# Performance work log

Hardware: AMD Instinct MI355X
Metric: run time of the kernel (lower is better)

Reference implementation:

```python
import jax, jax.numpy as jnp
from jax import lax
import numpy as np

T = 8
TAU = 2.0       # LIFNode tau
VTH = 1.0       # v_threshold for IF and LIF
ALPHA = 2.0     # surrogate.ATan default alpha
BN_EPS = 1e-5

# --- ATan surrogate-gradient heaviside (spikingjelly semantics) ---
@jax.custom_vjp
def heaviside_atan(x):
    return (x >= 0.0).astype(x.dtype)

def _h_fwd(x):
    return heaviside_atan(x), x

def _h_bwd(x, g):
    sg = (ALPHA / 2.0) / (1.0 + (jnp.pi / 2.0 * ALPHA * x) ** 2)
    return (g * sg,)

heaviside_atan.defvjp(_h_fwd, _h_bwd)

# --- multi-step IF node: v += x; spike; hard reset to 0 ---
def if_node(x_seq):
    def step(v, x):
        v = v + x
        s = heaviside_atan(v - VTH)
        return (1.0 - s) * v, s
    return lax.scan(step, jnp.zeros_like(x_seq[0]), x_seq)[1]

# --- multi-step LIF node (decay_input=True, v_reset=0, hard reset) ---
def lif_node(x_seq):
    def step(v, x):
        v = v + (x - v) / TAU
        s = heaviside_atan(v - VTH)
        return (1.0 - s) * v, s
    return lax.scan(step, jnp.zeros_like(x_seq[0]), x_seq)[1]

def conv2d(x, w, b):
    y = lax.conv_general_dilated(x, w, (1, 1), 'SAME', dimension_numbers=('NCHW', 'OIHW', 'NCHW'))
    return y + b[None, :, None, None]

def bn(x, g, b, m, v):
    scale = g * lax.rsqrt(v + BN_EPS)
    return (x - m[None, :, None, None]) * scale[None, :, None, None] + b[None, :, None, None]

def maxpool2(x):
    return lax.reduce_window(x, -jnp.inf, lax.max, (1, 1, 2, 2), (1, 1, 2, 2), 'VALID')


def setup_inputs():
    key = jax.random.key(0)
    ks = jax.random.split(key, 8)
    B = 32
    f32 = jnp.float32
    d = {}
    d['x'] = jax.random.normal(ks[0], (B, 1, 48, 48), f32)
    d['conv1_w'] = jax.random.normal(ks[1], (128, 1, 3, 3), f32) * 0.2
    d['conv1_b'] = jnp.zeros((128,), f32)
    d['bn1_g'] = jnp.ones((128,), f32)
    d['bn1_b'] = jnp.zeros((128,), f32)
    d['bn1_m'] = jnp.zeros((128,), f32)
    d['bn1_v'] = jnp.ones((128,), f32)
    d['conv2_w'] = jax.random.normal(ks[2], (128, 128, 3, 3), f32) * 0.03
    d['conv2_b'] = jnp.zeros((128,), f32)
    d['bn2_g'] = jnp.ones((128,), f32)
    d['bn2_b'] = jnp.zeros((128,), f32)
    d['bn2_m'] = jnp.zeros((128,), f32)
    d['bn2_v'] = jnp.ones((128,), f32)
    d['fc1_w'] = jax.random.normal(ks[3], (1152, 128 * 12 * 12), f32) * 0.007
    d['fc1_b'] = jnp.zeros((1152,), f32)
    d['fc2_w'] = jax.random.normal(ks[4], (128, 1152), f32) * 0.03
    d['fc2_b'] = jnp.zeros((128,), f32)
    d['fc3_w'] = jax.random.normal(ks[5], (7, 128), f32) * 0.09
    d['fc3_b'] = jnp.zeros((7,), f32)
    return d


def reference(x, conv1_w, conv1_b, bn1_g, bn1_b, bn1_m, bn1_v,
              conv2_w, conv2_b, bn2_g, bn2_b, bn2_m, bn2_v,
              fc1_w, fc1_b, fc2_w, fc2_b, fc3_w, fc3_b):
    B = x.shape[0]
    # layer1 (single-step): conv + BN (eval-mode), dropout is identity at eval
    h = bn(conv2d(x, conv1_w, conv1_b), bn1_g, bn1_b, bn1_m, bn1_v)  # [B,128,48,48]
    # repeat over T timesteps
    x_step = jnp.broadcast_to(h, (T,) + h.shape)                      # [T,B,128,48,48]
    # layer2: IF -> maxpool -> conv -> BN -> IF -> maxpool
    s1 = if_node(x_step)                                              # [T,B,128,48,48]
    p1 = maxpool2(s1.reshape((T * B,) + s1.shape[2:]))                # [T*B,128,24,24]
    c2 = bn(conv2d(p1, conv2_w, conv2_b), bn2_g, bn2_b, bn2_m, bn2_v)
    s2 = if_node(c2.reshape((T, B) + c2.shape[1:]))                   # [T,B,128,24,24]
    p2 = maxpool2(s2.reshape((T * B,) + s2.shape[2:]))                # [T*B,128,12,12]
    # layer3: flatten -> fc -> LIF -> fc -> LIF -> fc -> LIF
    f = p2.reshape(T, B, -1)                                          # [T,B,18432]
    l1 = lif_node(jnp.einsum('tbi,oi->tbo', f, fc1_w) + fc1_b)        # [T,B,1152]
    l2 = lif_node(jnp.einsum('tbi,oi->tbo', l1, fc2_w) + fc2_b)       # [T,B,128]
    l3 = lif_node(jnp.einsum('tbi,oi->tbo', l2, fc3_w) + fc3_b)       # [T,B,7]
    return l3.mean(axis=0)                                            # [B,7]
```

## Files before the change

### kernel.cpp

```cpp
#include <hip/hip_runtime.h>
#include <hip/hip_bf16.h>


typedef float  f32x4  __attribute__((ext_vector_type(4)));
typedef __bf16 bf16x8 __attribute__((ext_vector_type(8)));

#define T_STEPS 8

static const size_t OFF_P1    = 0;
static const size_t OFF_PART  = 0;
static const size_t OFF_WT    = 44302336;
static const size_t OFF_P2    = 45481984;
static const size_t OFF_W2T   = 54919168;
static const size_t OFF_L1S   = 55508992;

__device__ __forceinline__ unsigned short bf16_rne(float f) {
  unsigned u = __builtin_bit_cast(unsigned, f);
  u += 0x7FFFu + ((u >> 16) & 1u);
  return (unsigned short)(u >> 16);
}
__device__ __forceinline__ float bf16_to_f(unsigned short h) {
  unsigned u = ((unsigned)h) << 16;
  return __builtin_bit_cast(float, u);
}

__device__ __forceinline__ void split_pair(float f0, float f1, unsigned& hi, unsigned& lo) {
  __hip_bfloat162 h2 = __float22bfloat162_rn(make_float2(f0, f1));
  unsigned uh; __builtin_memcpy(&uh, &h2, 4);
  float g0 = __builtin_bit_cast(float, uh << 16);
  float g1 = __builtin_bit_cast(float, uh & 0xFFFF0000u);
  __hip_bfloat162 l2 = __float22bfloat162_rn(make_float2(f0 - g0, f1 - g1));
  unsigned ul; __builtin_memcpy(&ul, &l2, 4);
  hi = uh;
  lo = ul;
}

__device__ __forceinline__ void lds_load16(const void* g, void* l) {
  auto* gp = reinterpret_cast<const __attribute__((address_space(1))) unsigned int*>(
      reinterpret_cast<uintptr_t>(g));
  auto* lp = reinterpret_cast<__attribute__((address_space(3))) unsigned int*>(
      reinterpret_cast<uintptr_t>(l));
  __builtin_amdgcn_global_load_lds(gp, lp, 16, 0, 0);
}

__global__ __launch_bounds__(256) void prep(const float* __restrict__ conv2_w,
                                            const float* __restrict__ fc2_w,
                                            short* __restrict__ wt_hi,
                                            short* __restrict__ wt_lo,
                                            float* __restrict__ w2t,
                                            uint4* __restrict__ p1pad4) {
  int i = blockIdx.x * 256 + threadIdx.x;
  if (i < 147456) {
    int tap = i >> 14;
    int oc  = (i >> 7) & 127;
    int ic  = i & 127;
    float wv = conv2_w[oc * 1152 + ic * 9 + tap];
    unsigned short h = bf16_rne(wv);
    wt_hi[i] = (short)h;
    wt_lo[i] = (short)bf16_rne(wv - bf16_to_f(h));
  } else if (i < 294912) {
    int j = i - 147456;
    int o = j & 127, k = j >> 7;
    w2t[j] = fc2_w[o * 1152 + k];
  } else if (i < 704512) {
    int k = i - 294912;
    int tb = k / 1600;
    int rem = k - tb * 1600;
    int pos = rem >> 4, c8 = rem & 15;
    int y, x;
    if (pos < 26)      { y = 0;  x = pos; }
    else if (pos < 52) { y = 25; x = pos - 26; }
    else { int jj = pos - 52; y = 1 + (jj >> 1); x = (jj & 1) * 25; }
    p1pad4[(tb * 676 + y * 26 + x) * 16 + c8] = make_uint4(0u, 0u, 0u, 0u);
  }
}

__global__ __launch_bounds__(128) void conv1_if_pool(
    const float* __restrict__ x, const float* __restrict__ w1, const float* __restrict__ b1,
    const float* __restrict__ g1, const float* __restrict__ be1, const float* __restrict__ m1,
    const float* __restrict__ vv1, short* __restrict__ p1) {
  __shared__ float patch[16];
  const int c  = threadIdx.x;
  const int sp = blockIdx.x;
  const int b  = blockIdx.y;
  const int oy = sp / 24, ox = sp % 24;
  if (c < 16) {
    int py = c >> 2, px = c & 3;
    int iy = 2 * oy - 1 + py, ix = 2 * ox - 1 + px;
    float v = 0.f;
    if (iy >= 0 && iy < 48 && ix >= 0 && ix < 48) v = x[b * 2304 + iy * 48 + ix];
    patch[c] = v;
  }
  __syncthreads();
  float w[9];
#pragma unroll
  for (int i = 0; i < 9; ++i) w[i] = w1[c * 9 + i];
  float scale = g1[c] * rsqrtf(vv1[c] + 1e-5f);
  float shift = (b1[c] - m1[c]) * scale + be1[c];
  float h[4];
#pragma unroll
  for (int p = 0; p < 4; ++p) {
    int py = p >> 1, px = p & 1;
    float s = 0.f;
#pragma unroll
    for (int dy = 0; dy < 3; ++dy)
#pragma unroll
      for (int dx = 0; dx < 3; ++dx) s += patch[(py + dy) * 4 + (px + dx)] * w[dy * 3 + dx];
    h[p] = s * scale + shift;
  }
  float va = 0.f, vb = 0.f, vc = 0.f, vd = 0.f;
  size_t base = ((size_t)b * 676 + (size_t)(1 + oy) * 26 + (1 + ox)) * 128 + c;
#pragma unroll
  for (int t = 0; t < T_STEPS; ++t) {
    va += h[0]; vb += h[1]; vc += h[2]; vd += h[3];
    bool s0 = va >= 1.f, s1 = vb >= 1.f, s2 = vc >= 1.f, s3 = vd >= 1.f;
    p1[base + (size_t)t * (32 * 676 * 128)] = (s0 | s1 | s2 | s3) ? (short)0x3F80 : (short)0;
    if (s0) va = 0.f; if (s1) vb = 0.f; if (s2) vc = 0.f; if (s3) vd = 0.f;
  }
}

__global__ __launch_bounds__(256, 2) void conv2_gemm(
    const short* __restrict__ p1pad, const short* __restrict__ wt_hi, const short* __restrict__ wt_lo,
    const float* __restrict__ conv2_b, const float* __restrict__ bn2_g, const float* __restrict__ bn2_b,
    const float* __restrict__ bn2_m, const float* __restrict__ bn2_v, short* __restrict__ p2) {
  __shared__ __align__(16) short lds[32768];
  short* ldsA  = lds;
  short* ldsBh = lds + 16384;
  short* ldsBl = lds + 24576;

  const int tid = threadIdx.x;
  const int lane = tid & 63;
  const int w = tid >> 6;
  const int wm = w & 1, wn = w >> 1;
  const int b = blockIdx.y;
  const int gy = blockIdx.x / 3;
  const int gx = blockIdx.x - gy * 3;

  const int g = (lane & 7) ^ (lane >> 3);
  int rowofsA[8], bofs[4];
#pragma unroll
  for (int j = 0; j < 8; ++j) {
    int r = w * 64 + j * 8 + (lane >> 3);
    int t = r >> 5, iy = (r >> 3) & 3, ix = r & 7;
    rowofsA[j] = (((t * 32 + b) * 676) + (4 * gy + iy) * 26 + (8 * gx + ix)) * 128 + g * 8;
  }
#pragma unroll
  for (int j = 0; j < 4; ++j) {
    int n = w * 32 + j * 8 + (lane >> 3);
    bofs[j] = n * 128 + g * 8;
  }

  f32x4 acc[8][4];
#pragma unroll
  for (int mi = 0; mi < 8; ++mi)
#pragma unroll
    for (int ni = 0; ni < 4; ++ni) acc[mi][ni] = (f32x4){0.f, 0.f, 0.f, 0.f};

#pragma unroll 1
  for (int s = 0; s < 18; ++s) {
    const int tap = s >> 1;
    const int kk = (s & 1) << 6;
    const int tapoff = ((tap / 3) * 26 + (tap % 3)) * 128;
    __syncthreads();
#pragma unroll
    for (int j = 0; j < 8; ++j) {
      lds_load16(p1pad + rowofsA[j] + tapoff + kk, ldsA + (w * 64 + j * 8) * 64 + lane * 8);
    }
    const int wtoff = tap * 16384 + kk;
#pragma unroll
    for (int j = 0; j < 4; ++j) {
      lds_load16(wt_hi + wtoff + bofs[j], ldsBh + (w * 32 + j * 8) * 64 + lane * 8);
      lds_load16(wt_lo + wtoff + bofs[j], ldsBl + (w * 32 + j * 8) * 64 + lane * 8);
    }
    __syncthreads();
#pragma unroll
    for (int ks = 0; ks < 2; ++ks) {
      const int cch = ks * 4 + (lane >> 4);
      bf16x8 a[8], bh[4], bl[4];
#pragma unroll
      for (int i = 0; i < 8; ++i) {
        int r = wm * 128 + i * 16 + (lane & 15);
        a[i] = *(const bf16x8*)(ldsA + r * 64 + ((cch ^ (r & 7)) * 8));
      }
#pragma unroll
      for (int i = 0; i < 4; ++i) {
        int n = wn * 64 + i * 16 + (lane & 15);
        bh[i] = *(const bf16x8*)(ldsBh + n * 64 + ((cch ^ (n & 7)) * 8));
        bl[i] = *(const bf16x8*)(ldsBl + n * 64 + ((cch ^ (n & 7)) * 8));
      }
#pragma unroll
      for (int mi = 0; mi < 8; ++mi)
#pragma unroll
        for (int ni = 0; ni < 4; ++ni) {
          acc[mi][ni] = __builtin_amdgcn_mfma_f32_16x16x32_bf16(a[mi], bh[ni], acc[mi][ni], 0, 0, 0);
          acc[mi][ni] = __builtin_amdgcn_mfma_f32_16x16x32_bf16(a[mi], bl[ni], acc[mi][ni], 0, 0, 0);
        }
    }
  }

  float sc[4], sh[4];
#pragma unroll
  for (int ni = 0; ni < 4; ++ni) {
    int oc = wn * 64 + ni * 16 + (lane & 15);
    sc[ni] = bn2_g[oc] * rsqrtf(bn2_v[oc] + 1e-5f);
    sh[ni] = (conv2_b[oc] - bn2_m[oc]) * sc[ni] + bn2_b[oc];
  }
  float* ybuf = (float*)lds;
  const int S = 132;
  float v[32];
#pragma unroll
  for (int q = 0; q < 32; ++q) v[q] = 0.f;
  unsigned short* p2u = (unsigned short*)p2;
  __syncthreads();
#pragma unroll
  for (int q = 0; q < 4; ++q) {
    if (wm == (q >> 1)) {
      const int mib = (q & 1) * 4;
#pragma unroll
      for (int ml = 0; ml < 4; ++ml)
#pragma unroll
        for (int ni = 0; ni < 4; ++ni)
#pragma unroll
          for (int r = 0; r < 4; ++r) {
            int lam = ml * 16 + ((lane >> 4) << 2) + r;
            int col = wn * 64 + ni * 16 + (lane & 15);
            ybuf[lam * S + col] = acc[mib + ml][ni][r] * sc[ni] + sh[ni];
          }
    }
    __syncthreads();
    if (tid < 128) {
      const int oc = tid;
#pragma unroll
      for (int tt = 0; tt < 2; ++tt) {
        int t = 2 * q + tt;
#pragma unroll
        for (int pooly = 0; pooly < 2; ++pooly) {
          unsigned short ov[4];
#pragma unroll
          for (int poolx = 0; poolx < 4; ++poolx) {
            bool any = false;
#pragma unroll
            for (int ry = 0; ry < 2; ++ry)
#pragma unroll
              for (int rx = 0; rx < 2; ++rx) {
                int iy = 2 * pooly + ry, ix = 2 * poolx + rx;
                float xx = ybuf[(tt * 32 + iy * 8 + ix) * S + oc];
                int qi = iy * 8 + ix;
                v[qi] += xx;
                bool ss = v[qi] >= 1.f;
                any |= ss;
                if (ss) v[qi] = 0.f;
              }
            ov[poolx] = any ? (unsigned short)0x3F80 : (unsigned short)0;
          }
          ushort4 o4; o4.x = ov[0]; o4.y = ov[1]; o4.z = ov[2]; o4.w = ov[3];
          *(ushort4*)(p2u + ((size_t)(t * 32 + b) * 128 + oc) * 144 + (2 * gy + pooly) * 12 + 4 * gx) = o4;
        }
      }
    }
    __syncthreads();
  }
}

__global__ __launch_bounds__(512) void fc1_gemm(const short* __restrict__ p2,
                                                const float* __restrict__ fc1_w,
                                                float* __restrict__ part) {
  __shared__ __align__(16) short lds[32768];
  short* ldsA = lds;
  short* ldsBh = lds + 16384;
  short* ldsBl = lds + 24576;

  const int tid = threadIdx.x;
  const int lane = tid & 63;
  const int w = tid >> 6;
  const int wm = w & 3, wn = w >> 2;
  const int n0 = blockIdx.x * 128;
  const int kb = blockIdx.y * 576;

  const int g = (lane & 7) ^ (lane >> 3);
  int aofs[4];
#pragma unroll
  for (int j = 0; j < 4; ++j) {
    int r = w * 32 + j * 8 + (lane >> 3);
    aofs[j] = r * 18432 + g * 8;
  }
  const int bn = tid >> 2;
  const int c0 = (tid & 3) * 2;
  const float* wrow = fc1_w + (size_t)(n0 + bn) * 18432 + c0 * 8;
  const int bpos0 = (c0 ^ (bn & 7)) * 8;
  const int bpos1 = ((c0 + 1) ^ (bn & 7)) * 8;

  f32x4 acc[4][4];
#pragma unroll
  for (int mi = 0; mi < 4; ++mi)
#pragma unroll
    for (int ni = 0; ni < 4; ++ni) acc[mi][ni] = (f32x4){0.f, 0.f, 0.f, 0.f};

#pragma unroll 1
  for (int s = 0; s < 9; ++s) {
    const int koff = kb + s * 64;
    __syncthreads();
#pragma unroll
    for (int j = 0; j < 4; ++j) {
      lds_load16(p2 + aofs[j] + koff, ldsA + (w * 32 + j * 8) * 64 + lane * 8);
    }
    {
      const float4* wp = (const float4*)(wrow + koff);
      float4 q0 = wp[0], q1 = wp[1], q2 = wp[2], q3 = wp[3];
      unsigned h0, h1, h2, h3, h4, h5, h6, h7;
      unsigned l0, l1, l2, l3, l4, l5, l6, l7;
      split_pair(q0.x, q0.y, h0, l0);
      split_pair(q0.z, q0.w, h1, l1);
      split_pair(q1.x, q1.y, h2, l2);
      split_pair(q1.z, q1.w, h3, l3);
      split_pair(q2.x, q2.y, h4, l4);
      split_pair(q2.z, q2.w, h5, l5);
      split_pair(q3.x, q3.y, h6, l6);
      split_pair(q3.z, q3.w, h7, l7);
      uint4 H0; H0.x = h0; H0.y = h1; H0.z = h2; H0.w = h3;
      uint4 H1; H1.x = h4; H1.y = h5; H1.z = h6; H1.w = h7;
      uint4 L0; L0.x = l0; L0.y = l1; L0.z = l2; L0.w = l3;
      uint4 L1; L1.x = l4; L1.y = l5; L1.z = l6; L1.w = l7;
      *(uint4*)(ldsBh + bn * 64 + bpos0) = H0;
      *(uint4*)(ldsBh + bn * 64 + bpos1) = H1;
      *(uint4*)(ldsBl + bn * 64 + bpos0) = L0;
      *(uint4*)(ldsBl + bn * 64 + bpos1) = L1;
    }
    __syncthreads();
#pragma unroll
    for (int ks = 0; ks < 2; ++ks) {
      bf16x8 a[4], bh[4], bl[4];
      const int cch = ks * 4 + (lane >> 4);
#pragma unroll
      for (int i = 0; i < 4; ++i) {
        int r = wm * 64 + i * 16 + (lane & 15);
        a[i] = *(const bf16x8*)(ldsA + r * 64 + ((cch ^ (r & 7)) * 8));
        int n = wn * 64 + i * 16 + (lane & 15);
        bh[i] = *(const bf16x8*)(ldsBh + n * 64 + ((cch ^ (n & 7)) * 8));
        bl[i] = *(const bf16x8*)(ldsBl + n * 64 + ((cch ^ (n & 7)) * 8));
      }
#pragma unroll
      for (int mi = 0; mi < 4; ++mi)
#pragma unroll
        for (int ni = 0; ni < 4; ++ni) {
          acc[mi][ni] = __builtin_amdgcn_mfma_f32_16x16x32_bf16(a[mi], bh[ni], acc[mi][ni], 0, 0, 0);
          acc[mi][ni] = __builtin_amdgcn_mfma_f32_16x16x32_bf16(a[mi], bl[ni], acc[mi][ni], 0, 0, 0);
        }
    }
  }
  const size_t pbase = (size_t)(blockIdx.y * 9 + blockIdx.x) * 32768;
#pragma unroll
  for (int ni = 0; ni < 4; ++ni) {
    int j = wn * 64 + ni * 16 + (lane & 15);
#pragma unroll
    for (int mi = 0; mi < 4; ++mi) {
#pragma unroll
      for (int r = 0; r < 4; ++r) {
        int m = wm * 64 + mi * 16 + ((lane >> 4) << 2) + r;
        part[pbase + (size_t)m * 128 + j] = acc[mi][ni][r];
      }
    }
  }
}

__global__ __launch_bounds__(128) void fc1_reduce_lif(const float* __restrict__ part,
                                                      const float* __restrict__ fc1_b,
                                                      float* __restrict__ l1s) {
  int i = blockIdx.x * 128 + threadIdx.x;
  int b = i / 1152, n = i - b * 1152;
  int nt = n >> 7, j = n & 127;
  float bias = fc1_b[n];
  float v = 0.f;
#pragma unroll
  for (int t = 0; t < T_STEPS; ++t) {
    int m = t * 32 + b;
    float s = bias;
#pragma unroll 8
    for (int ks = 0; ks < 32; ++ks) s += part[(((size_t)ks * 9 + nt) * 256 + m) * 128 + j];
    v += (s - v) * 0.5f;
    bool sp = v >= 1.f;
    l1s[(size_t)m * 1152 + n] = sp ? 1.f : 0.f;
    if (sp) v = 0.f;
  }
}

__global__ __launch_bounds__(512) void tail(const float* __restrict__ l1s,
                                            const float* __restrict__ w2t,
                                            const float* __restrict__ b2,
                                            const float* __restrict__ w3,
                                            const float* __restrict__ b3,
                                            float* __restrict__ out) {
  __shared__ float sx[8][1152];
  __shared__ float part2[4][8][128];
  __shared__ float s2[8][128];
  __shared__ float y3[7][8];
  const int b = blockIdx.x;
  const int tid = threadIdx.x;
  for (int i = tid; i < 9216; i += 512) {
    int t = i / 1152, k = i - t * 1152;
    sx[t][k] = l1s[(size_t)(t * 32 + b) * 1152 + k];
  }
  __syncthreads();
  const int o = tid & 127, h = tid >> 7;
  float p[8];
#pragma unroll
  for (int t = 0; t < 8; ++t) p[t] = 0.f;
#pragma unroll 4
  for (int kk = 0; kk < 288; ++kk) {
    int k = h * 288 + kk;
    float wv = w2t[k * 128 + o];
#pragma unroll
    for (int t = 0; t < 8; ++t) p[t] += sx[t][k] * wv;
  }
#pragma unroll
  for (int t = 0; t < 8; ++t) part2[h][t][o] = p[t];
  __syncthreads();
  if (tid < 128) {
    float v = 0.f;
#pragma unroll
    for (int t = 0; t < 8; ++t) {
      float xx = part2[0][t][o] + part2[1][t][o] + part2[2][t][o] + part2[3][t][o] + b2[o];
      v += (xx - v) * 0.5f;
      bool s = v >= 1.f;
      s2[t][o] = s ? 1.f : 0.f;
      if (s) v = 0.f;
    }
  }
  __syncthreads();
  if (tid < 56) {
    int oo = tid >> 3, t = tid & 7;
    float d = 0.f;
    for (int k = 0; k < 128; ++k) d += s2[t][k] * w3[oo * 128 + k];
    y3[oo][t] = d + b3[oo];
  }
  __syncthreads();
  if (tid < 7) {
    float v = 0.f, a = 0.f;
#pragma unroll
    for (int t = 0; t < 8; ++t) {
      float xx = y3[tid][t];
      v += (xx - v) * 0.5f;
      bool s = v >= 1.f;
      a += s ? 1.f : 0.f;
      if (s) v = 0.f;
    }
    out[b * 7 + tid] = a * 0.125f;
  }
}

extern "C" void kernel_launch(void* const* d_in, const int* in_sizes, int n_in,
                              void* d_out, int out_size, void* d_ws, size_t ws_size,
                              hipStream_t stream) {
  const float* x       = (const float*)d_in[0];
  const float* conv1_w = (const float*)d_in[1];
  const float* conv1_b = (const float*)d_in[2];
  const float* bn1_g   = (const float*)d_in[3];
  const float* bn1_b   = (const float*)d_in[4];
  const float* bn1_m   = (const float*)d_in[5];
  const float* bn1_v   = (const float*)d_in[6];
  const float* conv2_w = (const float*)d_in[7];
  const float* conv2_b = (const float*)d_in[8];
  const float* bn2_g   = (const float*)d_in[9];
  const float* bn2_b   = (const float*)d_in[10];
  const float* bn2_m   = (const float*)d_in[11];
  const float* bn2_v   = (const float*)d_in[12];
  const float* fc1_w   = (const float*)d_in[13];
  const float* fc1_b   = (const float*)d_in[14];
  const float* fc2_w   = (const float*)d_in[15];
  const float* fc2_b   = (const float*)d_in[16];
  const float* fc3_w   = (const float*)d_in[17];
  const float* fc3_b   = (const float*)d_in[18];

  char* ws = (char*)d_ws;
  short* p1pad = (short*)(ws + OFF_P1);
  float* part  = (float*)(ws + OFF_PART);
  short* wt_hi = (short*)(ws + OFF_WT);
  short* wt_lo = wt_hi + 147456;
  short* p2    = (short*)(ws + OFF_P2);
  float* w2t   = (float*)(ws + OFF_W2T);
  float* l1s   = (float*)(ws + OFF_L1S);
  float* out   = (float*)d_out;

  prep<<<2752, 256, 0, stream>>>(conv2_w, fc2_w, wt_hi, wt_lo, w2t, (uint4*)p1pad);
  conv1_if_pool<<<dim3(576, 32), 128, 0, stream>>>(x, conv1_w, conv1_b, bn1_g, bn1_b, bn1_m, bn1_v, p1pad);
  conv2_gemm<<<dim3(18, 32), 256, 0, stream>>>(p1pad, wt_hi, wt_lo, conv2_b, bn2_g, bn2_b, bn2_m, bn2_v, p2);
  fc1_gemm<<<dim3(9, 32), 512, 0, stream>>>(p2, fc1_w, part);
  fc1_reduce_lif<<<288, 128, 0, stream>>>(part, fc1_b, l1s);
  tail<<<32, 512, 0, stream>>>(l1s, w2t, fc2_b, fc3_w, fc3_b, out);
}
```

Baseline: 367.3 us.

## Shrink conv2 GEMM tile and K-step to raise occupancy and block count

```diff
diff --git a/kernel.cpp b/kernel.cpp
--- a/kernel.cpp
+++ b/kernel.cpp
@@ -119,14 +119,14 @@
   }
 }
 
-__global__ __launch_bounds__(256, 2) void conv2_gemm(
+__global__ __launch_bounds__(256, 4) void conv2_gemm(
     const short* __restrict__ p1pad, const short* __restrict__ wt_hi, const short* __restrict__ wt_lo,
     const float* __restrict__ conv2_b, const float* __restrict__ bn2_g, const float* __restrict__ bn2_b,
     const float* __restrict__ bn2_m, const float* __restrict__ bn2_v, short* __restrict__ p2) {
-  __shared__ __align__(16) short lds[32768];
+  __shared__ __align__(16) short lds[12288];
   short* ldsA  = lds;
-  short* ldsBh = lds + 16384;
-  short* ldsBl = lds + 24576;
+  short* ldsBh = lds + 4096;
+  short* ldsBl = lds + 8192;
 
   const int tid = threadIdx.x;
   const int lane = tid & 63;
@@ -136,66 +136,55 @@
   const int gy = blockIdx.x / 3;
   const int gx = blockIdx.x - gy * 3;
 
-  const int g = (lane & 7) ^ (lane >> 3);
-  int rowofsA[8], bofs[4];
-#pragma unroll
-  for (int j = 0; j < 8; ++j) {
-    int r = w * 64 + j * 8 + (lane >> 3);
-    int t = r >> 5, iy = (r >> 3) & 3, ix = r & 7;
-    rowofsA[j] = (((t * 32 + b) * 676) + (4 * gy + iy) * 26 + (8 * gx + ix)) * 128 + g * 8;
-  }
-#pragma unroll
-  for (int j = 0; j < 4; ++j) {
-    int n = w * 32 + j * 8 + (lane >> 3);
-    bofs[j] = n * 128 + g * 8;
-  }
-
-  f32x4 acc[8][4];
-#pragma unroll
-  for (int mi = 0; mi < 8; ++mi)
+  int rowofsA[2], bofs[2];
+#pragma unroll
+  for (int j = 0; j < 2; ++j) {
+    int r = j * 64 + w * 16 + (lane >> 2);
+    int t = r >> 4, iy = (r >> 3) & 1, ix = r & 7;
+    rowofsA[j] = (((t * 32 + b) * 676) + (2 * gy + iy) * 26 + (8 * gx + ix)) * 128 + (lane & 3) * 8;
+    bofs[j] = r * 128 + (lane & 3) * 8;
+  }
+
+  f32x4 acc[4][4];
+#pragma unroll
+  for (int mi = 0; mi < 4; ++mi)
 #pragma unroll
     for (int ni = 0; ni < 4; ++ni) acc[mi][ni] = (f32x4){0.f, 0.f, 0.f, 0.f};
 
 #pragma unroll 1
-  for (int s = 0; s < 18; ++s) {
-    const int tap = s >> 1;
-    const int kk = (s & 1) << 6;
+  for (int s = 0; s < 36; ++s) {
+    const int tap = s >> 2;
+    const int kk = (s & 3) << 5;
     const int tapoff = ((tap / 3) * 26 + (tap % 3)) * 128;
     __syncthreads();
 #pragma unroll
-    for (int j = 0; j < 8; ++j) {
-      lds_load16(p1pad + rowofsA[j] + tapoff + kk, ldsA + (w * 64 + j * 8) * 64 + lane * 8);
+    for (int j = 0; j < 2; ++j) {
+      lds_load16(p1pad + rowofsA[j] + tapoff + kk, ldsA + (j * 64 + w * 16) * 32 + lane * 8);
     }
     const int wtoff = tap * 16384 + kk;
 #pragma unroll
-    for (int j = 0; j < 4; ++j) {
-      lds_load16(wt_hi + wtoff + bofs[j], ldsBh + (w * 32 + j * 8) * 64 + lane * 8);
-      lds_load16(wt_lo + wtoff + bofs[j], ldsBl + (w * 32 + j * 8) * 64 + lane * 8);
-    }
-    __syncthreads();
-#pragma unroll
-    for (int ks = 0; ks < 2; ++ks) {
-      const int cch = ks * 4 + (lane >> 4);
-      bf16x8 a[8], bh[4], bl[4];
-#pragma unroll
-      for (int i = 0; i < 8; ++i) {
-        int r = wm * 128 + i * 16 + (lane & 15);
-        a[i] = *(const bf16x8*)(ldsA + r * 64 + ((cch ^ (r & 7)) * 8));
+    for (int j = 0; j < 2; ++j) {
+      lds_load16(wt_hi + wtoff + bofs[j], ldsBh + (j * 64 + w * 16) * 32 + lane * 8);
+      lds_load16(wt_lo + wtoff + bofs[j], ldsBl + (j * 64 + w * 16) * 32 + lane * 8);
+    }
+    __syncthreads();
+    const int cch = lane >> 4;
+    bf16x8 a[4], bh[4], bl[4];
+#pragma unroll
+    for (int i = 0; i < 4; ++i) {
+      int r = wm * 64 + i * 16 + (lane & 15);
+      a[i] = *(const bf16x8*)(ldsA + r * 32 + cch * 8);
+      int n = wn * 64 + i * 16 + (lane & 15);
+      bh[i] = *(const bf16x8*)(ldsBh + n * 32 + cch * 8);
+      bl[i] = *(const bf16x8*)(ldsBl + n * 32 + cch * 8);
+    }
+#pragma unroll
+    for (int mi = 0; mi < 4; ++mi)
+#pragma unroll
+      for (int ni = 0; ni < 4; ++ni) {
+        acc[mi][ni] = __builtin_amdgcn_mfma_f32_16x16x32_bf16(a[mi], bh[ni], acc[mi][ni], 0, 0, 0);
+        acc[mi][ni] = __builtin_amdgcn_mfma_f32_16x16x32_bf16(a[mi], bl[ni], acc[mi][ni], 0, 0, 0);
       }
-#pragma unroll
-      for (int i = 0; i < 4; ++i) {
-        int n = wn * 64 + i * 16 + (lane & 15);
-        bh[i] = *(const bf16x8*)(ldsBh + n * 64 + ((cch ^ (n & 7)) * 8));
-        bl[i] = *(const bf16x8*)(ldsBl + n * 64 + ((cch ^ (n & 7)) * 8));
-      }
-#pragma unroll
-      for (int mi = 0; mi < 8; ++mi)
-#pragma unroll
-        for (int ni = 0; ni < 4; ++ni) {
-          acc[mi][ni] = __builtin_amdgcn_mfma_f32_16x16x32_bf16(a[mi], bh[ni], acc[mi][ni], 0, 0, 0);
-          acc[mi][ni] = __builtin_amdgcn_mfma_f32_16x16x32_bf16(a[mi], bl[ni], acc[mi][ni], 0, 0, 0);
-        }
-    }
   }
 
   float sc[4], sh[4];
@@ -207,25 +196,26 @@
   }
   float* ybuf = (float*)lds;
   const int S = 132;
-  float v[32];
-#pragma unroll
-  for (int q = 0; q < 32; ++q) v[q] = 0.f;
+  float v[16];
+#pragma unroll
+  for (int q = 0; q < 16; ++q) v[q] = 0.f;
   unsigned short* p2u = (unsigned short*)p2;
   __syncthreads();
 #pragma unroll
   for (int q = 0; q < 4; ++q) {
     if (wm == (q >> 1)) {
-      const int mib = (q & 1) * 4;
-#pragma unroll
-      for (int ml = 0; ml < 4; ++ml)
+#pragma unroll
+      for (int ml = 0; ml < 2; ++ml) {
+        const int mi = (q & 1) * 2 + ml;
 #pragma unroll
         for (int ni = 0; ni < 4; ++ni)
 #pragma unroll
           for (int r = 0; r < 4; ++r) {
             int lam = ml * 16 + ((lane >> 4) << 2) + r;
             int col = wn * 64 + ni * 16 + (lane & 15);
-            ybuf[lam * S + col] = acc[mib + ml][ni][r] * sc[ni] + sh[ni];
+            ybuf[lam * S + col] = acc[mi][ni][r] * sc[ni] + sh[ni];
           }
+      }
     }
     __syncthreads();
     if (tid < 128) {
@@ -233,29 +223,25 @@
 #pragma unroll
       for (int tt = 0; tt < 2; ++tt) {
         int t = 2 * q + tt;
-#pragma unroll
-        for (int pooly = 0; pooly < 2; ++pooly) {
-          unsigned short ov[4];
-#pragma unroll
-          for (int poolx = 0; poolx < 4; ++poolx) {
-            bool any = false;
-#pragma unroll
-            for (int ry = 0; ry < 2; ++ry)
-#pragma unroll
-              for (int rx = 0; rx < 2; ++rx) {
-                int iy = 2 * pooly + ry, ix = 2 * poolx + rx;
-                float xx = ybuf[(tt * 32 + iy * 8 + ix) * S + oc];
-                int qi = iy * 8 + ix;
-                v[qi] += xx;
-                bool ss = v[qi] >= 1.f;
-                any |= ss;
-                if (ss) v[qi] = 0.f;
-              }
-            ov[poolx] = any ? (unsigned short)0x3F80 : (unsigned short)0;
-          }
-          ushort4 o4; o4.x = ov[0]; o4.y = ov[1]; o4.z = ov[2]; o4.w = ov[3];
-          *(ushort4*)(p2u + ((size_t)(t * 32 + b) * 128 + oc) * 144 + (2 * gy + pooly) * 12 + 4 * gx) = o4;
+        unsigned short ov[4];
+#pragma unroll
+        for (int px = 0; px < 4; ++px) {
+          bool any = false;
+#pragma unroll
+          for (int iy = 0; iy < 2; ++iy)
+#pragma unroll
+            for (int rx = 0; rx < 2; ++rx) {
+              int pos = iy * 8 + 2 * px + rx;
+              float xx = ybuf[(tt * 16 + pos) * S + oc];
+              v[pos] += xx;
+              bool ss = v[pos] >= 1.f;
+              any |= ss;
+              if (ss) v[pos] = 0.f;
+            }
+          ov[px] = any ? (unsigned short)0x3F80 : (unsigned short)0;
         }
+        ushort4 o4; o4.x = ov[0]; o4.y = ov[1]; o4.z = ov[2]; o4.w = ov[3];
+        *(ushort4*)(p2u + ((size_t)(t * 32 + b) * 128 + oc) * 144 + gy * 12 + gx * 4) = o4;
       }
     }
     __syncthreads();
@@ -483,7 +469,7 @@
 
   prep<<<2752, 256, 0, stream>>>(conv2_w, fc2_w, wt_hi, wt_lo, w2t, (uint4*)p1pad);
   conv1_if_pool<<<dim3(576, 32), 128, 0, stream>>>(x, conv1_w, conv1_b, bn1_g, bn1_b, bn1_m, bn1_v, p1pad);
-  conv2_gemm<<<dim3(18, 32), 256, 0, stream>>>(p1pad, wt_hi, wt_lo, conv2_b, bn2_g, bn2_b, bn2_m, bn2_v, p2);
+  conv2_gemm<<<dim3(36, 32), 256, 0, stream>>>(p1pad, wt_hi, wt_lo, conv2_b, bn2_g, bn2_b, bn2_m, bn2_v, p2);
   fc1_gemm<<<dim3(9, 32), 512, 0, stream>>>(p2, fc1_w, part);
   fc1_reduce_lif<<<288, 128, 0, stream>>>(part, fc1_b, l1s);
   tail<<<32, 512, 0, stream>>>(l1s, w2t, fc2_b, fc3_w, fc3_b, out);
```

Result: slower. 378.6 us (+3.1%).
